# Performance work log

Measured on AMD Instinct MI355X. Metric: run time of the kernel, lower is better.

Reference implementation:

```python
import jax, jax.numpy as jnp
import numpy as np
import math

B, T, C, H = 4, 2048, 1024, 16
HD = C // H  # head_size = 64


def setup_inputs() -> dict:
    key = jax.random.key(0)
    ks = jax.random.split(key, 8)
    s = 1.0 / math.sqrt(C)
    inp = {
        "v": jax.random.normal(ks[0], (B, T, C), jnp.float32),
        "k": jax.random.normal(ks[1], (B, T, C), jnp.float32),
        "q": jax.random.normal(ks[2], (B, T, C), jnp.float32),
        # causal mask, broadcastable over batch and heads; 0 -> masked
        "mask": jnp.tril(jnp.ones((T, T), jnp.int32))[None, None, :, :],
        # nn.Linear weights stored [out, in] as in torch
        "Wk": jax.random.normal(ks[3], (C, C), jnp.float32) * s,
        "Wq": jax.random.normal(ks[4], (C, C), jnp.float32) * s,
        "Wv": jax.random.normal(ks[5], (C, C), jnp.float32) * s,
        "Wo": jax.random.normal(ks[6], (C, C), jnp.float32) * s,
        "bo": jax.random.normal(ks[7], (C,), jnp.float32) * s,
    }
    return inp


def reference(v, k, q, mask, Wk, Wq, Wv, Wo, bo):
    b, t, c = q.shape
    # linear projections (torch: y = x @ W.T)
    kp = jnp.einsum("btc,dc->btd", k, Wk).reshape(b, t, H, HD).transpose(0, 2, 1, 3)
    qp = jnp.einsum("btc,dc->btd", q, Wq).reshape(b, t, H, HD).transpose(0, 2, 1, 3)
    vp = jnp.einsum("btc,dc->btd", v, Wv).reshape(b, t, H, HD).transpose(0, 2, 1, 3)
    # NOTE: source scales by 1/sqrt(k.size(0)) == 1/sqrt(batch) (faithful)
    scale = 1.0 / math.sqrt(b)
    score = jnp.einsum("bhqd,bhkd->bhqk", qp, kp) * scale  # [B,H,T,T]
    score = jnp.where(mask == 0, -jnp.inf, score)
    score = jax.nn.softmax(score, axis=-1)
    out = jnp.einsum("bhqk,bhkd->bhqd", score, vp)  # [B,H,T,HD]
    out = out.transpose(0, 2, 1, 3).reshape(b, t, c)
    out = jnp.einsum("btc,dc->btd", out, Wo) + bo  # dropout = identity (eval)
    return out
```

## Files before the change

### kernel.cpp

```cpp
#include <hip/hip_runtime.h>
#include <stdint.h>

#define BB 4
#define TT 2048
#define CC 1024
#define HH 16
#define DD 64
#define MM (BB*TT)

typedef unsigned short u16;
typedef unsigned int   u32;
typedef __attribute__((ext_vector_type(8))) __bf16 bf16x8;
typedef __attribute__((ext_vector_type(4))) float  f32x4;

typedef __attribute__((address_space(1))) const u32 as1_u32;
typedef __attribute__((address_space(3))) u32       as3_u32;

__device__ __forceinline__ u16 f2b(float f) {
    u32 u = __builtin_bit_cast(u32, f);
    u32 r = u + 0x7FFFu + ((u >> 16) & 1u);
    return (u16)(r >> 16);
}

__device__ __forceinline__ f32x4 mfma16(uint4 a, uint4 b, f32x4 c) {
    return __builtin_amdgcn_mfma_f32_16x16x32_bf16(
        __builtin_bit_cast(bf16x8, a), __builtin_bit_cast(bf16x8, b), c, 0, 0, 0);
}

__device__ __forceinline__ void glds16(const u16* g, u16* l) {
    __builtin_amdgcn_global_load_lds((const as1_u32*)g, (as3_u32*)l, 16, 0, 0);
}

__global__ __launch_bounds__(256) void cvt_kernel(const float* __restrict__ s,
                                                  u16* __restrict__ d, int n) {
    int i = (blockIdx.x * 256 + threadIdx.x) * 4;
    if (i < n) {
        float4 v = *(const float4*)(s + i);
        ushort4 o;
        o.x = f2b(v.x); o.y = f2b(v.y); o.z = f2b(v.z); o.w = f2b(v.w);
        *(ushort4*)(d + i) = o;
    }
}

template<int MODE>
__global__ __launch_bounds__(256, 2)
void gemm_bt(const u16* __restrict__ A, const u16* __restrict__ Bw,
             const float* __restrict__ bias, void* __restrict__ Out, float scale) {
    __shared__ u16 As[128 * 32];
    __shared__ u16 Bs[128 * 32];

    const int tid  = threadIdx.x;
    const int lane = tid & 63;
    const int wv   = tid >> 6;
    const int m0   = blockIdx.x * 128;
    const int n0   = blockIdx.y * 128;
    const int wm   = (wv & 1) * 64;
    const int wn   = (wv >> 1) * 64;
    const int fr   = lane & 15;
    const int fg   = lane >> 4;

    const int srow = wv * 16 + (lane >> 2);
    const int sel  = (lane & 3) * 8;

    const u16* gA0 = A  + (size_t)(m0 + srow) * CC + sel;
    const u16* gA1 = gA0 + (size_t)64 * CC;
    const u16* gB0 = Bw + (size_t)(n0 + srow) * CC + sel;
    const u16* gB1 = gB0 + (size_t)64 * CC;
    u16* sA0 = As + wv * 512;
    u16* sA1 = As + 2048 + wv * 512;
    u16* sB0 = Bs + wv * 512;
    u16* sB1 = Bs + 2048 + wv * 512;

    f32x4 acc[4][4] = {};

    for (int k0 = 0; k0 < CC; k0 += 32) {
        glds16(gA0 + k0, sA0);
        glds16(gA1 + k0, sA1);
        glds16(gB0 + k0, sB0);
        glds16(gB1 + k0, sB1);
        __syncthreads();
        uint4 af[4], bfr[4];
#pragma unroll
        for (int i = 0; i < 4; ++i)
            af[i] = *(const uint4*)(As + (wm + i * 16 + fr) * 32 + fg * 8);
#pragma unroll
        for (int i = 0; i < 4; ++i)
            bfr[i] = *(const uint4*)(Bs + (wn + i * 16 + fr) * 32 + fg * 8);
#pragma unroll
        for (int mi = 0; mi < 4; ++mi)
#pragma unroll
            for (int ni = 0; ni < 4; ++ni)
                acc[mi][ni] = mfma16(af[mi], bfr[ni], acc[mi][ni]);
        __syncthreads();
    }

    if constexpr (MODE == 0) {
        u16* O = (u16*)Out;
#pragma unroll
        for (int mi = 0; mi < 4; ++mi)
#pragma unroll
            for (int r = 0; r < 4; ++r) {
                int m = m0 + wm + mi * 16 + fg * 4 + r;
                size_t base = (size_t)m * CC + n0 + wn + fr;
#pragma unroll
                for (int ni = 0; ni < 4; ++ni)
                    O[base + ni * 16] = f2b(acc[mi][ni][r] * scale);
            }
    } else if constexpr (MODE == 1) {
        u16* O = (u16*)Out;
#pragma unroll
        for (int mi = 0; mi < 4; ++mi) {
            int m  = m0 + wm + mi * 16 + fg * 4;
            int b_ = m >> 11;
            int t0 = m & 2047;
            int blk = t0 >> 6;
            int tl  = t0 & 63;
            int pbase = (blk << 6) + ((tl & 15) << 2) + (tl >> 4);
#pragma unroll
            for (int ni = 0; ni < 4; ++ni) {
                int n = n0 + wn + ni * 16 + fr;
                u16* orow = O + ((size_t)b_ * CC + n) * TT;
#pragma unroll
                for (int r = 0; r < 4; ++r)
                    orow[pbase + 4 * r] = f2b(acc[mi][ni][r] * scale);
            }
        }
    } else {
        float* O = (float*)Out;
#pragma unroll
        for (int mi = 0; mi < 4; ++mi)
#pragma unroll
            for (int r = 0; r < 4; ++r) {
                int m = m0 + wm + mi * 16 + fg * 4 + r;
                size_t base = (size_t)m * CC + n0 + wn + fr;
#pragma unroll
                for (int ni = 0; ni < 4; ++ni)
                    O[base + ni * 16] = acc[mi][ni][r] + bias[n0 + wn + ni * 16 + fr];
            }
    }
}

__global__ __launch_bounds__(256, 2)
void flash_attn(const u16* __restrict__ Qp, const u16* __restrict__ Kp,
                const u16* __restrict__ Vt, u16* __restrict__ Att) {
    __shared__ u16 Qs[128 * 72];
    __shared__ u16 Ks[64 * 72];
    __shared__ u16 Vs[64 * 72];
    __shared__ u16 Ps[4 * 32 * 72];

    const int tid = threadIdx.x, lane = tid & 63, wv = tid >> 6;
    const int fr = lane & 15, fg = lane >> 4;
    const int bh = blockIdx.y;
    const int b = bh >> 4, h = bh & 15;
    u16* pw = Ps + wv * 32 * 72;
    const uint4 ONES = {0x3F803F80u, 0x3F803F80u, 0x3F803F80u, 0x3F803F80u};

    for (int half = 0; half < 2; ++half) {
        const int qi = half ? (15 - (int)blockIdx.x) : (int)blockIdx.x;
        const int q0 = qi * 128;

#pragma unroll
        for (int i = 0; i < 4; ++i) {
            int ch = i * 256 + tid;
            int r = ch >> 3, cp = (ch & 7) * 8;
            *(uint4*)(Qs + r * 72 + cp) =
                *(const uint4*)(Qp + ((size_t)(b * TT + q0 + r)) * CC + h * 64 + cp);
        }
        __syncthreads();

        uint4 qf[2][2];
#pragma unroll
        for (int mi = 0; mi < 2; ++mi)
#pragma unroll
            for (int ks = 0; ks < 2; ++ks)
                qf[mi][ks] = *(const uint4*)(Qs + (wv * 32 + mi * 16 + fr) * 72 + ks * 32 + fg * 8);

        f32x4 oacc[2][4] = {};
        f32x4 lacc[2] = {};

        const int nkt = 2 * (qi + 1);
        for (int kt = 0; kt < nkt; ++kt) {
            const int k0 = kt * 64;
#pragma unroll
            for (int i = 0; i < 2; ++i) {
                int ch = i * 256 + tid;
                int r = ch >> 3, cp = (ch & 7) * 8;
                *(uint4*)(Ks + r * 72 + cp) =
                    *(const uint4*)(Kp + ((size_t)(b * TT + k0 + r)) * CC + h * 64 + cp);
                *(uint4*)(Vs + r * 72 + cp) =
                    *(const uint4*)(Vt + ((size_t)(bh * 64 + r)) * TT + k0 + cp);
            }
            __syncthreads();

            uint4 kf[4][2];
#pragma unroll
            for (int ni = 0; ni < 4; ++ni)
#pragma unroll
                for (int ks = 0; ks < 2; ++ks)
                    kf[ni][ks] = *(const uint4*)(Ks + (ni * 16 + fr) * 72 + ks * 32 + fg * 8);
            f32x4 s[2][4];
#pragma unroll
            for (int mi = 0; mi < 2; ++mi)
#pragma unroll
                for (int ni = 0; ni < 4; ++ni) {
                    f32x4 a = {0.f, 0.f, 0.f, 0.f};
                    a = mfma16(qf[mi][0], kf[ni][0], a);
                    a = mfma16(qf[mi][1], kf[ni][1], a);
                    s[mi][ni] = a;
                }

            if (k0 + 63 > q0 + wv * 32) {
#pragma unroll
                for (int mi = 0; mi < 2; ++mi)
#pragma unroll
                    for (int r = 0; r < 4; ++r) {
                        int tq = q0 + wv * 32 + mi * 16 + fg * 4 + r;
#pragma unroll
                        for (int ni = 0; ni < 4; ++ni) {
                            int tk = k0 + ni * 16 + fr;
                            if (tk > tq) s[mi][ni][r] = -1e30f;
                        }
                    }
            }

#pragma unroll
            for (int mi = 0; mi < 2; ++mi)
#pragma unroll
                for (int r = 0; r < 4; ++r) {
                    float p0 = __builtin_amdgcn_exp2f(s[mi][0][r]);
                    float p1 = __builtin_amdgcn_exp2f(s[mi][1][r]);
                    float p2 = __builtin_amdgcn_exp2f(s[mi][2][r]);
                    float p3 = __builtin_amdgcn_exp2f(s[mi][3][r]);
                    u32 d0 = (u32)f2b(p0) | ((u32)f2b(p1) << 16);
                    u32 d1 = (u32)f2b(p2) | ((u32)f2b(p3) << 16);
                    uint2 dd = {d0, d1};
                    *(uint2*)(pw + (mi * 16 + fg * 4 + r) * 72 + fr * 4) = dd;
                }

            uint4 vf[4][2];
#pragma unroll
            for (int ni = 0; ni < 4; ++ni)
#pragma unroll
                for (int ks = 0; ks < 2; ++ks)
                    vf[ni][ks] = *(const uint4*)(Vs + (ni * 16 + fr) * 72 + ks * 32 + fg * 8);
#pragma unroll
            for (int mi = 0; mi < 2; ++mi) {
                uint4 pf0 = *(const uint4*)(pw + (mi * 16 + fr) * 72 + fg * 8);
                uint4 pf1 = *(const uint4*)(pw + (mi * 16 + fr) * 72 + 32 + fg * 8);
                lacc[mi] = mfma16(pf0, ONES, lacc[mi]);
                lacc[mi] = mfma16(pf1, ONES, lacc[mi]);
#pragma unroll
                for (int ni = 0; ni < 4; ++ni) {
                    oacc[mi][ni] = mfma16(pf0, vf[ni][0], oacc[mi][ni]);
                    oacc[mi][ni] = mfma16(pf1, vf[ni][1], oacc[mi][ni]);
                }
            }
            __syncthreads();
        }

#pragma unroll
        for (int mi = 0; mi < 2; ++mi)
#pragma unroll
            for (int r = 0; r < 4; ++r) {
                float inv = 1.0f / lacc[mi][r];
                int t = q0 + wv * 32 + mi * 16 + fg * 4 + r;
                size_t base = ((size_t)(b * TT + t)) * CC + h * 64 + fr;
#pragma unroll
                for (int ni = 0; ni < 4; ++ni)
                    Att[base + ni * 16] = f2b(oacc[mi][ni][r] * inv);
            }
    }
}

extern "C" void kernel_launch(void* const* d_in, const int* in_sizes, int n_in,
                              void* d_out, int out_size, void* d_ws, size_t ws_size,
                              hipStream_t stream) {
    (void)in_sizes; (void)n_in; (void)out_size; (void)ws_size;
    const float* v  = (const float*)d_in[0];
    const float* k  = (const float*)d_in[1];
    const float* q  = (const float*)d_in[2];
    const float* Wk = (const float*)d_in[4];
    const float* Wq = (const float*)d_in[5];
    const float* Wv = (const float*)d_in[6];
    const float* Wo = (const float*)d_in[7];
    const float* bo = (const float*)d_in[8];

    char* ws = (char*)d_ws;
    const size_t SI = (size_t)MM * CC * 2;
    const size_t SW = (size_t)CC * CC * 2;
    u16* qb  = (u16*)(ws + 0 * SI);
    u16* kb  = (u16*)(ws + 1 * SI);
    u16* vb  = (u16*)(ws + 2 * SI);
    u16* Qp  = (u16*)(ws + 3 * SI);
    u16* Kp  = (u16*)(ws + 4 * SI);
    u16* Vtp = (u16*)(ws + 5 * SI);
    u16* wq  = (u16*)(ws + 6 * SI + 0 * SW);
    u16* wk  = (u16*)(ws + 6 * SI + 1 * SW);
    u16* wvv = (u16*)(ws + 6 * SI + 2 * SW);
    u16* wo  = (u16*)(ws + 6 * SI + 3 * SW);
    u16* att = qb;

    const int nin = MM * CC;
    const int nw  = CC * CC;
    cvt_kernel<<<nin / 1024, 256, 0, stream>>>(q, qb, nin);
    cvt_kernel<<<nin / 1024, 256, 0, stream>>>(k, kb, nin);
    cvt_kernel<<<nin / 1024, 256, 0, stream>>>(v, vb, nin);
    cvt_kernel<<<nw / 1024, 256, 0, stream>>>(Wq, wq, nw);
    cvt_kernel<<<nw / 1024, 256, 0, stream>>>(Wk, wk, nw);
    cvt_kernel<<<nw / 1024, 256, 0, stream>>>(Wv, wvv, nw);
    cvt_kernel<<<nw / 1024, 256, 0, stream>>>(Wo, wo, nw);

    const float csc = 0.5f * 1.44269504088896f;
    dim3 gg(MM / 128, CC / 128);
    gemm_bt<0><<<gg, 256, 0, stream>>>(qb, wq, nullptr, Qp, csc);
    gemm_bt<0><<<gg, 256, 0, stream>>>(kb, wk, nullptr, Kp, 1.0f);
    gemm_bt<1><<<gg, 256, 0, stream>>>(vb, wvv, nullptr, Vtp, 1.0f);
    flash_attn<<<dim3(8, 64), 256, 0, stream>>>(Qp, Kp, Vtp, att);
    gemm_bt<2><<<gg, 256, 0, stream>>>(att, wo, bo, d_out, 1.0f);
}
```

Baseline: 343.5 us.

## Double GEMM K-tile to 64 with XOR-swizzled LDS and batch conversion launches

```diff
diff --git a/kernel.cpp b/kernel.cpp
--- a/kernel.cpp
+++ b/kernel.cpp
@@ -31,8 +31,16 @@
     __builtin_amdgcn_global_load_lds((const as1_u32*)g, (as3_u32*)l, 16, 0, 0);
 }
 
-__global__ __launch_bounds__(256) void cvt_kernel(const float* __restrict__ s,
-                                                  u16* __restrict__ d, int n) {
+__global__ __launch_bounds__(256) void cvt3_kernel(const float* __restrict__ s0,
+                                                   const float* __restrict__ s1,
+                                                   const float* __restrict__ s2,
+                                                   u16* __restrict__ d0,
+                                                   u16* __restrict__ d1,
+                                                   u16* __restrict__ d2, int n) {
+    const float* s; u16* d;
+    if (blockIdx.y == 0)      { s = s0; d = d0; }
+    else if (blockIdx.y == 1) { s = s1; d = d1; }
+    else                      { s = s2; d = d2; }
     int i = (blockIdx.x * 256 + threadIdx.x) * 4;
     if (i < n) {
         float4 v = *(const float4*)(s + i);
@@ -42,12 +50,34 @@
     }
 }
 
+__global__ __launch_bounds__(256) void cvt4_kernel(const float* __restrict__ s0,
+                                                   const float* __restrict__ s1,
+                                                   const float* __restrict__ s2,
+                                                   const float* __restrict__ s3,
+                                                   u16* __restrict__ d0,
+                                                   u16* __restrict__ d1,
+                                                   u16* __restrict__ d2,
+                                                   u16* __restrict__ d3, int n) {
+    const float* s; u16* d;
+    if (blockIdx.y == 0)      { s = s0; d = d0; }
+    else if (blockIdx.y == 1) { s = s1; d = d1; }
+    else if (blockIdx.y == 2) { s = s2; d = d2; }
+    else                      { s = s3; d = d3; }
+    int i = (blockIdx.x * 256 + threadIdx.x) * 4;
+    if (i < n) {
+        float4 v = *(const float4*)(s + i);
+        ushort4 o;
+        o.x = f2b(v.x); o.y = f2b(v.y); o.z = f2b(v.z); o.w = f2b(v.w);
+        *(ushort4*)(d + i) = o;
+    }
+}
+
 template<int MODE>
 __global__ __launch_bounds__(256, 2)
 void gemm_bt(const u16* __restrict__ A, const u16* __restrict__ Bw,
              const float* __restrict__ bias, void* __restrict__ Out, float scale) {
-    __shared__ u16 As[128 * 32];
-    __shared__ u16 Bs[128 * 32];
+    __shared__ u16 As[128 * 64];
+    __shared__ u16 Bs[128 * 64];
 
     const int tid  = threadIdx.x;
     const int lane = tid & 63;
@@ -58,40 +88,40 @@
     const int wn   = (wv >> 1) * 64;
     const int fr   = lane & 15;
     const int fg   = lane >> 4;
-
-    const int srow = wv * 16 + (lane >> 2);
-    const int sel  = (lane & 3) * 8;
-
-    const u16* gA0 = A  + (size_t)(m0 + srow) * CC + sel;
-    const u16* gA1 = gA0 + (size_t)64 * CC;
-    const u16* gB0 = Bw + (size_t)(n0 + srow) * CC + sel;
-    const u16* gB1 = gB0 + (size_t)64 * CC;
-    u16* sA0 = As + wv * 512;
-    u16* sA1 = As + 2048 + wv * 512;
-    u16* sB0 = Bs + wv * 512;
-    u16* sB1 = Bs + 2048 + wv * 512;
+    const int xsw  = fr & 7;
+
+    const int lrow = lane >> 3;
+    const int lcol = (((lane & 7) ^ lrow) * 8);
+    const u16* gA = A  + (size_t)(m0 + wv * 32 + lrow) * CC + lcol;
+    const u16* gB = Bw + (size_t)(n0 + wv * 32 + lrow) * CC + lcol;
+    u16* sA = As + (wv * 32) * 64;
+    u16* sB = Bs + (wv * 32) * 64;
 
     f32x4 acc[4][4] = {};
 
-    for (int k0 = 0; k0 < CC; k0 += 32) {
-        glds16(gA0 + k0, sA0);
-        glds16(gA1 + k0, sA1);
-        glds16(gB0 + k0, sB0);
-        glds16(gB1 + k0, sB1);
+    for (int k0 = 0; k0 < CC; k0 += 64) {
         __syncthreads();
-        uint4 af[4], bfr[4];
-#pragma unroll
-        for (int i = 0; i < 4; ++i)
-            af[i] = *(const uint4*)(As + (wm + i * 16 + fr) * 32 + fg * 8);
-#pragma unroll
-        for (int i = 0; i < 4; ++i)
-            bfr[i] = *(const uint4*)(Bs + (wn + i * 16 + fr) * 32 + fg * 8);
-#pragma unroll
-        for (int mi = 0; mi < 4; ++mi)
-#pragma unroll
-            for (int ni = 0; ni < 4; ++ni)
-                acc[mi][ni] = mfma16(af[mi], bfr[ni], acc[mi][ni]);
+#pragma unroll
+        for (int j = 0; j < 4; ++j) {
+            glds16(gA + (size_t)j * 8 * CC + k0, sA + j * 512);
+            glds16(gB + (size_t)j * 8 * CC + k0, sB + j * 512);
+        }
         __syncthreads();
+#pragma unroll
+        for (int ks = 0; ks < 2; ++ks) {
+            uint4 af[4], bfr[4];
+#pragma unroll
+            for (int i = 0; i < 4; ++i) {
+                int ca = ((ks * 4 + fg) ^ xsw) * 8;
+                af[i]  = *(const uint4*)(As + (wm + i * 16 + fr) * 64 + ca);
+                bfr[i] = *(const uint4*)(Bs + (wn + i * 16 + fr) * 64 + ca);
+            }
+#pragma unroll
+            for (int mi = 0; mi < 4; ++mi)
+#pragma unroll
+                for (int ni = 0; ni < 4; ++ni)
+                    acc[mi][ni] = mfma16(af[mi], bfr[ni], acc[mi][ni]);
+        }
     }
 
     if constexpr (MODE == 0) {
@@ -302,13 +332,8 @@
 
     const int nin = MM * CC;
     const int nw  = CC * CC;
-    cvt_kernel<<<nin / 1024, 256, 0, stream>>>(q, qb, nin);
-    cvt_kernel<<<nin / 1024, 256, 0, stream>>>(k, kb, nin);
-    cvt_kernel<<<nin / 1024, 256, 0, stream>>>(v, vb, nin);
-    cvt_kernel<<<nw / 1024, 256, 0, stream>>>(Wq, wq, nw);
-    cvt_kernel<<<nw / 1024, 256, 0, stream>>>(Wk, wk, nw);
-    cvt_kernel<<<nw / 1024, 256, 0, stream>>>(Wv, wvv, nw);
-    cvt_kernel<<<nw / 1024, 256, 0, stream>>>(Wo, wo, nw);
+    cvt3_kernel<<<dim3(nin / 1024, 3), 256, 0, stream>>>(q, k, v, qb, kb, vb, nin);
+    cvt4_kernel<<<dim3(nw / 1024, 4), 256, 0, stream>>>(Wq, Wk, Wv, Wo, wq, wk, wvv, wo, nw);
 
     const float csc = 0.5f * 1.44269504088896f;
     dim3 gg(MM / 128, CC / 128);
```

New measurement: 315.3 us. 1.09x faster.
